# Optimization experiments

Hardware: AMD Instinct MI355X
Metric: run time of the kernel (lower is better)

## Reference

```python
import jax, jax.numpy as jnp
import numpy as np

B, S, D = 4, 2048, 1024


def setup_inputs() -> dict:
    key = jax.random.key(0)
    k1, k2, k3, k4 = jax.random.split(key, 4)
    x = jax.random.normal(k1, (B, S, D), dtype=jnp.float32)
    # 'random_normal' keras initializer uses stddev=0.05
    w_keys = jax.random.normal(k2, (D, D), dtype=jnp.float32) * 0.05
    w_queries = jax.random.normal(k3, (D, D), dtype=jnp.float32) * 0.05
    w_values = jax.random.normal(k4, (D, D), dtype=jnp.float32) * 0.05
    return {"x": x, "w_keys": w_keys, "w_queries": w_queries, "w_values": w_values}


def reference(x, w_keys, w_queries, w_values):
    # fact = sqrt(input feature dim)
    fact = jnp.sqrt(jnp.asarray(x.shape[-1], x.dtype))
    vk = x @ w_keys      # [B,S,D]
    vq = x @ w_queries   # [B,S,D]
    vv = x @ w_values    # [B,S,D]
    # NOTE: module computes K @ Q^T (keys as rows), softmax over last axis
    kq = jnp.einsum('bsd,btd->bst', vk, vq) / fact   # [B,S,S]
    sn = jax.nn.softmax(kq, axis=-1)
    # pm + transpose_b cancel: out = sn @ vv
    out = jnp.einsum('bst,btd->bsd', sn, vv)         # [B,S,D]
    return out
```

## Files before the change

kernel.cpp:

```cpp
#include <hip/hip_runtime.h>


typedef __attribute__((ext_vector_type(8))) short bf16x8;
typedef __attribute__((ext_vector_type(4))) float f32x4;

__device__ __forceinline__ unsigned short f2bf(float f) {
    unsigned int u = __float_as_uint(f);
    u += 0x7fff + ((u >> 16) & 1);
    return (unsigned short)(u >> 16);
}
__device__ __forceinline__ float bf2f(unsigned short s) {
    return __uint_as_float((unsigned int)s << 16);
}

__device__ __forceinline__ void gld_lds16(const unsigned short* g, unsigned short* l) {
    __builtin_amdgcn_global_load_lds(
        (const __attribute__((address_space(1))) void*)g,
        (__attribute__((address_space(3))) void*)l, 16, 0, 0);
}

template<int N> __device__ __forceinline__ void vmcnt_wait() {
    if constexpr (N == 0) asm volatile("s_waitcnt vmcnt(0)" ::: "memory");
    else if constexpr (N == 3) asm volatile("s_waitcnt vmcnt(3)" ::: "memory");
    else if constexpr (N == 4) asm volatile("s_waitcnt vmcnt(4)" ::: "memory");
}
__device__ __forceinline__ void bar() {
    asm volatile("" ::: "memory");
    __builtin_amdgcn_s_barrier();
    asm volatile("" ::: "memory");
}

template<int BN, int KT, bool RS>
__device__ __forceinline__ void gemm8(
    const unsigned short* __restrict__ A, const unsigned short* __restrict__ B,
    int lda, int ldb, int bm, int bn,
    unsigned short* As, unsigned short* Bs,
    f32x4 (&acc)[8][BN/64], float (&rs)[8])
{
    constexpr int NFR = BN / 64, NH = NFR / 2, LB = BN / 128;
    const int tid  = threadIdx.x;
    const int lane = tid & 63;
    const int wave = tid >> 6;
    const int wr = wave >> 2, wc = wave & 3;
    const int lr = lane & 15, kg = lane >> 4;

    const int srow = tid >> 2;
    const int soff = ((tid & 3) ^ ((tid >> 3) & 3)) * 8;
    const unsigned short* pa0 = A + (size_t)(bm + srow) * lda + soff;
    const unsigned short* pa1 = A + (size_t)(bm + 128 + srow) * lda + soff;
    const unsigned short* pb0 = B + (size_t)(bn + srow) * ldb + soff;
    const unsigned short* pb1 = B + (size_t)(bn + 128 + srow) * ldb + soff;

    const int runit = (kg ^ ((lr >> 1) & 3)) * 8;
    const int arow  = (wr * 128 + lr) * 32 + runit;
    const int brow  = (wc * (BN / 4) + lr) * 32 + runit;

    auto stageA = [&](int buf, int kt, int kh) {
        unsigned short* d = As + buf * 16384 + kh * 8192 + wave * 512;
        const int off = kt * 64 + kh * 32;
        gld_lds16(pa0 + off, d);
        gld_lds16(pa1 + off, d + 4096);
    };
    auto stageB = [&](int buf, int kt, int kh) {
        unsigned short* d = Bs + buf * (BN * 64) + kh * (BN * 32) + wave * 512;
        const int off = kt * 64 + kh * 32;
        gld_lds16(pb0 + off, d);
        if constexpr (BN == 256) gld_lds16(pb1 + off, d + 4096);
    };

    stageA(0, 0, 0); stageB(0, 0, 0); stageA(0, 0, 1); stageB(0, 0, 1);
    vmcnt_wait<0>();
    bar();

    for (int kt = 0; kt < KT; ++kt) {
        const int c = kt & 1, n = c ^ 1;
        const bool last = (kt == KT - 1);
        const unsigned short* Ab = As + c * 16384 + arow;
        const unsigned short* Bb = Bs + c * (BN * 64) + brow;

        bf16x8 af[8], bfr[NH];
        #pragma unroll
        for (int mf = 0; mf < 8; mf++) af[mf] = *reinterpret_cast<const bf16x8*>(Ab + mf * 512);
        #pragma unroll
        for (int j = 0; j < NH; j++) bfr[j] = *reinterpret_cast<const bf16x8*>(Bb + j * 512);
        if (!last) stageA(n, kt + 1, 0);
        bar();
        __builtin_amdgcn_s_setprio(1);
        #pragma unroll
        for (int mf = 0; mf < 8; mf++)
            #pragma unroll
            for (int j = 0; j < NH; j++)
                acc[mf][j] = __builtin_amdgcn_mfma_f32_16x16x32_bf16(af[mf], bfr[j], acc[mf][j], 0, 0, 0);
        __builtin_amdgcn_s_setprio(0);
        if constexpr (RS) {
            #pragma unroll
            for (int mf = 0; mf < 8; mf++)
                #pragma unroll
                for (int e = 0; e < 8; e++) rs[mf] += bf2f(((unsigned short*)&af[mf])[e]);
        }
        bar();

        #pragma unroll
        for (int j = 0; j < NH; j++) bfr[j] = *reinterpret_cast<const bf16x8*>(Bb + (NH + j) * 512);
        if (!last) stageB(n, kt + 1, 0);
        if (last) vmcnt_wait<0>(); else vmcnt_wait<2 + LB>();
        bar();
        __builtin_amdgcn_s_setprio(1);
        #pragma unroll
        for (int mf = 0; mf < 8; mf++)
            #pragma unroll
            for (int j = 0; j < NH; j++)
                acc[mf][NH + j] = __builtin_amdgcn_mfma_f32_16x16x32_bf16(af[mf], bfr[j], acc[mf][NH + j], 0, 0, 0);
        __builtin_amdgcn_s_setprio(0);
        bar();

        #pragma unroll
        for (int mf = 0; mf < 8; mf++) af[mf] = *reinterpret_cast<const bf16x8*>(Ab + 8192 + mf * 512);
        #pragma unroll
        for (int j = 0; j < NH; j++) bfr[j] = *reinterpret_cast<const bf16x8*>(Bb + BN * 32 + j * 512);
        if (!last) stageA(n, kt + 1, 1);
        bar();
        __builtin_amdgcn_s_setprio(1);
        #pragma unroll
        for (int mf = 0; mf < 8; mf++)
            #pragma unroll
            for (int j = 0; j < NH; j++)
                acc[mf][j] = __builtin_amdgcn_mfma_f32_16x16x32_bf16(af[mf], bfr[j], acc[mf][j], 0, 0, 0);
        __builtin_amdgcn_s_setprio(0);
        if constexpr (RS) {
            #pragma unroll
            for (int mf = 0; mf < 8; mf++)
                #pragma unroll
                for (int e = 0; e < 8; e++) rs[mf] += bf2f(((unsigned short*)&af[mf])[e]);
        }
        bar();

        #pragma unroll
        for (int j = 0; j < NH; j++) bfr[j] = *reinterpret_cast<const bf16x8*>(Bb + BN * 32 + (NH + j) * 512);
        if (!last) { stageB(n, kt + 1, 1); vmcnt_wait<2 + LB>(); }
        bar();
        __builtin_amdgcn_s_setprio(1);
        #pragma unroll
        for (int mf = 0; mf < 8; mf++)
            #pragma unroll
            for (int j = 0; j < NH; j++)
                acc[mf][NH + j] = __builtin_amdgcn_mfma_f32_16x16x32_bf16(af[mf], bfr[j], acc[mf][NH + j], 0, 0, 0);
        __builtin_amdgcn_s_setprio(0);
        bar();
    }
}

__global__ __launch_bounds__(256) void convert_x(
    const float* __restrict__ x, unsigned short* __restrict__ xb)
{
    const size_t idx = (size_t)blockIdx.x * 256 + threadIdx.x;
    const float4* xi = reinterpret_cast<const float4*>(x) + idx * 2;
    float4 v0 = xi[0], v1 = xi[1];
    ushort4 a = { f2bf(v0.x), f2bf(v0.y), f2bf(v0.z), f2bf(v0.w) };
    ushort4 b = { f2bf(v1.x), f2bf(v1.y), f2bf(v1.z), f2bf(v1.w) };
    ushort4* xo = reinterpret_cast<ushort4*>(xb) + idx * 2;
    xo[0] = a; xo[1] = b;
}

__global__ __launch_bounds__(256) void transpose_w(
    const float* __restrict__ w0, const float* __restrict__ w1, const float* __restrict__ w2,
    unsigned short* __restrict__ wT)
{
    __shared__ unsigned short T[64][72];
    const int z = blockIdx.z;
    const float* w = (z == 0) ? w0 : (z == 1 ? w1 : w2);
    unsigned short* o = wT + (size_t)z * 1024 * 1024;
    const int k0 = blockIdx.y * 64, n0 = blockIdx.x * 64;
    const int tid = threadIdx.x;
    const int r = tid >> 4, c4 = (tid & 15) * 4;
    #pragma unroll
    for (int i = 0; i < 4; i++) {
        int kr = r + i * 16;
        float4 v = *reinterpret_cast<const float4*>(&w[(size_t)(k0 + kr) * 1024 + n0 + c4]);
        T[c4 + 0][kr] = f2bf(v.x);
        T[c4 + 1][kr] = f2bf(v.y);
        T[c4 + 2][kr] = f2bf(v.z);
        T[c4 + 3][kr] = f2bf(v.w);
    }
    __syncthreads();
    #pragma unroll
    for (int i = 0; i < 4; i++) {
        int n = r + i * 16;
        ushort4 v = *reinterpret_cast<const ushort4*>(&T[n][c4]);
        *reinterpret_cast<ushort4*>(&o[(size_t)(n0 + n) * 1024 + k0 + c4]) = v;
    }
}

__global__ __launch_bounds__(512, 2) void proj_gemm(
    const unsigned short* __restrict__ xb, const unsigned short* __restrict__ wT,
    unsigned short* __restrict__ vk, unsigned short* __restrict__ vq,
    unsigned short* __restrict__ vvT)
{
    __shared__ unsigned short As[2 * 256 * 64], Bs[2 * 128 * 64];
    const int bid = blockIdx.x;
    const int wg  = (bid & 7) * 96 + (bid >> 3);
    const int z   = wg >> 8;
    const int rem = wg & 255;
    const int bm  = (rem >> 3) * 256;
    const int bn  = (rem & 7) * 128;
    const unsigned short* Bw = wT + (size_t)z * 1024 * 1024;

    f32x4 acc[8][2] = {};
    float rs[8] = {};
    gemm8<128, 16, false>(xb, Bw, 1024, 1024, bm, bn, As, Bs, acc, rs);

    const int tid = threadIdx.x, lane = tid & 63, wave = tid >> 6;
    const int wr = wave >> 2, wc = wave & 3, lr = lane & 15, kg = lane >> 4;
    if (z < 2) {
        unsigned short* out = z ? vq : vk;
        #pragma unroll
        for (int mf = 0; mf < 8; mf++)
            #pragma unroll
            for (int nf = 0; nf < 2; nf++)
                #pragma unroll
                for (int r = 0; r < 4; r++)
                    out[(size_t)(bm + wr * 128 + mf * 16 + kg * 4 + r) * 1024
                        + bn + wc * 32 + nf * 16 + lr] = f2bf(acc[mf][nf][r]);
    } else {
        const int batch = bm >> 11;
        unsigned short* o = vvT + (size_t)batch * 1024 * 2048;
        #pragma unroll
        for (int mf = 0; mf < 8; mf++)
            #pragma unroll
            for (int nf = 0; nf < 2; nf++) {
                ushort4 v = { f2bf(acc[mf][nf][0]), f2bf(acc[mf][nf][1]),
                              f2bf(acc[mf][nf][2]), f2bf(acc[mf][nf][3]) };
                *reinterpret_cast<ushort4*>(
                    &o[(size_t)(bn + wc * 32 + nf * 16 + lr) * 2048
                       + (bm & 2047) + wr * 128 + mf * 16 + kg * 4]) = v;
            }
    }
}

__global__ __launch_bounds__(512, 2) void scores_gemm(
    const unsigned short* __restrict__ vk, const unsigned short* __restrict__ vq,
    unsigned short* __restrict__ P)
{
    __shared__ unsigned short As[2 * 256 * 64], Bs[2 * 256 * 64];
    const int bid = blockIdx.x;
    const int wg  = (bid & 7) * 32 + (bid >> 3);
    const int z   = wg >> 6;
    const int rem = wg & 63;
    const int bm  = (rem >> 3) * 256;
    const int bn  = (rem & 7) * 256;
    const unsigned short* A = vk + (size_t)z * 2048 * 1024;
    const unsigned short* B = vq + (size_t)z * 2048 * 1024;
    unsigned short* out = P + (size_t)z * 2048 * 2048;

    f32x4 acc[8][4] = {};
    float rs[8] = {};
    gemm8<256, 16, false>(A, B, 1024, 1024, bm, bn, As, Bs, acc, rs);

    const int tid = threadIdx.x, lane = tid & 63, wave = tid >> 6;
    const int wr = wave >> 2, wc = wave & 3, lr = lane & 15, kg = lane >> 4;
    #pragma unroll
    for (int mf = 0; mf < 8; mf++)
        #pragma unroll
        for (int nf = 0; nf < 4; nf++)
            #pragma unroll
            for (int r = 0; r < 4; r++)
                out[(size_t)(bm + wr * 128 + mf * 16 + kg * 4 + r) * 2048
                    + bn + wc * 64 + nf * 16 + lr]
                    = f2bf(__expf(acc[mf][nf][r] * 0.03125f));
}

__global__ __launch_bounds__(512, 2) void pv_gemm(
    const unsigned short* __restrict__ P, const unsigned short* __restrict__ vvT,
    float* __restrict__ out)
{
    __shared__ unsigned short As[2 * 256 * 64], Bs[2 * 128 * 64];
    const int bid = blockIdx.x;
    const int wg  = (bid & 7) * 32 + (bid >> 3);
    const int z   = wg >> 6;
    const int rem = wg & 63;
    const int bm  = (rem >> 3) * 256;
    const int bn  = (rem & 7) * 128;
    const unsigned short* A = P   + (size_t)z * 2048 * 2048;
    const unsigned short* B = vvT + (size_t)z * 1024 * 2048;
    float* o = out + (size_t)z * 2048 * 1024;

    f32x4 acc[8][2] = {};
    float rs[8] = {};
    gemm8<128, 32, true>(A, B, 2048, 2048, bm, bn, As, Bs, acc, rs);

    const int tid = threadIdx.x, lane = tid & 63, wave = tid >> 6;
    const int wr = wave >> 2, wc = wave & 3, lr = lane & 15, kg = lane >> 4;

    #pragma unroll
    for (int mf = 0; mf < 8; mf++) {
        rs[mf] += __shfl_xor(rs[mf], 16);
        rs[mf] += __shfl_xor(rs[mf], 32);
    }
    #pragma unroll
    for (int mf = 0; mf < 8; mf++)
        #pragma unroll
        for (int r = 0; r < 4; r++) {
            const float l = __shfl(rs[mf], kg * 4 + r);
            const float inv = 1.0f / l;
            #pragma unroll
            for (int nf = 0; nf < 2; nf++)
                o[(size_t)(bm + wr * 128 + mf * 16 + kg * 4 + r) * 1024
                  + bn + wc * 32 + nf * 16 + lr] = acc[mf][nf][r] * inv;
        }
}

extern "C" void kernel_launch(void* const* d_in, const int* in_sizes, int n_in,
                              void* d_out, int out_size, void* d_ws, size_t ws_size,
                              hipStream_t stream) {
    const float* x  = (const float*)d_in[0];
    const float* wk = (const float*)d_in[1];
    const float* wq = (const float*)d_in[2];
    const float* wv = (const float*)d_in[3];
    float* out = (float*)d_out;

    char* ws = (char*)d_ws;
    const size_t MB = 1024 * 1024;
    unsigned short* xb  = (unsigned short*)(ws);
    unsigned short* wT  = (unsigned short*)(ws + 16 * MB);
    unsigned short* P   = (unsigned short*)(ws);
    unsigned short* vk  = (unsigned short*)(ws + 64 * MB);
    unsigned short* vq  = (unsigned short*)(ws + 80 * MB);
    unsigned short* vvT = (unsigned short*)(ws + 96 * MB);

    convert_x  <<<dim3(4096),      256, 0, stream>>>(x, xb);
    transpose_w<<<dim3(16, 16, 3), 256, 0, stream>>>(wk, wq, wv, wT);
    proj_gemm  <<<dim3(768),       512, 0, stream>>>(xb, wT, vk, vq, vvT);
    scores_gemm<<<dim3(256),       512, 0, stream>>>(vk, vq, P);
    pv_gemm    <<<dim3(256),       512, 0, stream>>>(P, vvT, out);
}
```

Baseline: 191.7 us.

## Restructure GEMM mainloop to prefetch two k-tiles ahead with fewer barriers

Replaces the four-phase interleaved mainloop, which had separate A/B staging and a barrier around every MFMA quarter, with a single stage call per k-step that loads both A and B. The tile for kt+2 is prefetched into the buffer just consumed, and only the kt+1 tile is waited on. This reduces the barrier count per k-step from eight to two and deepens the effective global-load lookahead. In exchange, all B fragments are held at once, which raises register pressure, and the global loads issue in bursts instead of being spread between MFMA groups.

```diff
diff --git a/kernel.cpp b/kernel.cpp
--- a/kernel.cpp
+++ b/kernel.cpp
@@ -21,8 +21,11 @@
 
 template<int N> __device__ __forceinline__ void vmcnt_wait() {
     if constexpr (N == 0) asm volatile("s_waitcnt vmcnt(0)" ::: "memory");
-    else if constexpr (N == 3) asm volatile("s_waitcnt vmcnt(3)" ::: "memory");
-    else if constexpr (N == 4) asm volatile("s_waitcnt vmcnt(4)" ::: "memory");
+    else if constexpr (N == 6) asm volatile("s_waitcnt vmcnt(6)" ::: "memory");
+    else if constexpr (N == 8) asm volatile("s_waitcnt vmcnt(8)" ::: "memory");
+}
+__device__ __forceinline__ void lgkm0() {
+    asm volatile("s_waitcnt lgkmcnt(0)" ::: "memory");
 }
 __device__ __forceinline__ void bar() {
     asm volatile("" ::: "memory");
@@ -37,7 +40,9 @@
     unsigned short* As, unsigned short* Bs,
     f32x4 (&acc)[8][BN/64], float (&rs)[8])
 {
-    constexpr int NFR = BN / 64, NH = NFR / 2, LB = BN / 128;
+    constexpr int NFR = BN / 64;
+    constexpr int LB  = BN / 128;
+    constexpr int L   = 4 + 2 * LB;
     const int tid  = threadIdx.x;
     const int lane = tid & 63;
     const int wave = tid >> 6;
@@ -55,97 +60,63 @@
     const int arow  = (wr * 128 + lr) * 32 + runit;
     const int brow  = (wc * (BN / 4) + lr) * 32 + runit;
 
-    auto stageA = [&](int buf, int kt, int kh) {
-        unsigned short* d = As + buf * 16384 + kh * 8192 + wave * 512;
-        const int off = kt * 64 + kh * 32;
-        gld_lds16(pa0 + off, d);
-        gld_lds16(pa1 + off, d + 4096);
+    auto stage = [&](int buf, int kt) {
+        unsigned short* da = As + buf * 16384 + wave * 512;
+        unsigned short* db = Bs + buf * (BN * 64) + wave * 512;
+        const int o0 = kt * 64, o1 = kt * 64 + 32;
+        gld_lds16(pa0 + o0, da);
+        gld_lds16(pa1 + o0, da + 4096);
+        gld_lds16(pa0 + o1, da + 8192);
+        gld_lds16(pa1 + o1, da + 8192 + 4096);
+        gld_lds16(pb0 + o0, db);
+        if constexpr (BN == 256) gld_lds16(pb1 + o0, db + 4096);
+        gld_lds16(pb0 + o1, db + BN * 32);
+        if constexpr (BN == 256) gld_lds16(pb1 + o1, db + BN * 32 + 4096);
     };
-    auto stageB = [&](int buf, int kt, int kh) {
-        unsigned short* d = Bs + buf * (BN * 64) + kh * (BN * 32) + wave * 512;
-        const int off = kt * 64 + kh * 32;
-        gld_lds16(pb0 + off, d);
-        if constexpr (BN == 256) gld_lds16(pb1 + off, d + 4096);
-    };
-
-    stageA(0, 0, 0); stageB(0, 0, 0); stageA(0, 0, 1); stageB(0, 0, 1);
-    vmcnt_wait<0>();
+
+    stage(0, 0);
+    stage(1, 1);
+    vmcnt_wait<L>();
     bar();
 
     for (int kt = 0; kt < KT; ++kt) {
-        const int c = kt & 1, n = c ^ 1;
-        const bool last = (kt == KT - 1);
+        const int c = kt & 1;
         const unsigned short* Ab = As + c * 16384 + arow;
         const unsigned short* Bb = Bs + c * (BN * 64) + brow;
 
-        bf16x8 af[8], bfr[NH];
-        #pragma unroll
-        for (int mf = 0; mf < 8; mf++) af[mf] = *reinterpret_cast<const bf16x8*>(Ab + mf * 512);
-        #pragma unroll
-        for (int j = 0; j < NH; j++) bfr[j] = *reinterpret_cast<const bf16x8*>(Bb + j * 512);
-        if (!last) stageA(n, kt + 1, 0);
-        bar();
-        __builtin_amdgcn_s_setprio(1);
-        #pragma unroll
-        for (int mf = 0; mf < 8; mf++)
-            #pragma unroll
-            for (int j = 0; j < NH; j++)
-                acc[mf][j] = __builtin_amdgcn_mfma_f32_16x16x32_bf16(af[mf], bfr[j], acc[mf][j], 0, 0, 0);
-        __builtin_amdgcn_s_setprio(0);
-        if constexpr (RS) {
+        #pragma unroll
+        for (int kk = 0; kk < 2; kk++) {
+            bf16x8 af[8], bfr[NFR];
+            #pragma unroll
+            for (int mf = 0; mf < 8; mf++)
+                af[mf] = *reinterpret_cast<const bf16x8*>(Ab + kk * 8192 + mf * 512);
+            #pragma unroll
+            for (int nf = 0; nf < NFR; nf++)
+                bfr[nf] = *reinterpret_cast<const bf16x8*>(Bb + kk * BN * 32 + nf * 512);
+            __builtin_amdgcn_s_setprio(1);
             #pragma unroll
             for (int mf = 0; mf < 8; mf++)
                 #pragma unroll
-                for (int e = 0; e < 8; e++) rs[mf] += bf2f(((unsigned short*)&af[mf])[e]);
+                for (int nf = 0; nf < NFR; nf++)
+                    acc[mf][nf] = __builtin_amdgcn_mfma_f32_16x16x32_bf16(af[mf], bfr[nf], acc[mf][nf], 0, 0, 0);
+            __builtin_amdgcn_s_setprio(0);
+            if constexpr (RS) {
+                #pragma unroll
+                for (int mf = 0; mf < 8; mf++)
+                    #pragma unroll
+                    for (int e = 0; e < 8; e++) rs[mf] += bf2f(((unsigned short*)&af[mf])[e]);
+            }
         }
+
+        if (kt == KT - 1) break;
+        lgkm0();
         bar();
-
-        #pragma unroll
-        for (int j = 0; j < NH; j++) bfr[j] = *reinterpret_cast<const bf16x8*>(Bb + (NH + j) * 512);
-        if (!last) stageB(n, kt + 1, 0);
-        if (last) vmcnt_wait<0>(); else vmcnt_wait<2 + LB>();
-        bar();
-        __builtin_amdgcn_s_setprio(1);
-        #pragma unroll
-        for (int mf = 0; mf < 8; mf++)
-            #pragma unroll
-            for (int j = 0; j < NH; j++)
-                acc[mf][NH + j] = __builtin_amdgcn_mfma_f32_16x16x32_bf16(af[mf], bfr[j], acc[mf][NH + j], 0, 0, 0);
-        __builtin_amdgcn_s_setprio(0);
-        bar();
-
-        #pragma unroll
-        for (int mf = 0; mf < 8; mf++) af[mf] = *reinterpret_cast<const bf16x8*>(Ab + 8192 + mf * 512);
-        #pragma unroll
-        for (int j = 0; j < NH; j++) bfr[j] = *reinterpret_cast<const bf16x8*>(Bb + BN * 32 + j * 512);
-        if (!last) stageA(n, kt + 1, 1);
-        bar();
-        __builtin_amdgcn_s_setprio(1);
-        #pragma unroll
-        for (int mf = 0; mf < 8; mf++)
-            #pragma unroll
-            for (int j = 0; j < NH; j++)
-                acc[mf][j] = __builtin_amdgcn_mfma_f32_16x16x32_bf16(af[mf], bfr[j], acc[mf][j], 0, 0, 0);
-        __builtin_amdgcn_s_setprio(0);
-        if constexpr (RS) {
-            #pragma unroll
-            for (int mf = 0; mf < 8; mf++)
-                #pragma unroll
-                for (int e = 0; e < 8; e++) rs[mf] += bf2f(((unsigned short*)&af[mf])[e]);
+        if (kt + 2 < KT) {
+            stage(c, kt + 2);
+            vmcnt_wait<L>();
+        } else {
+            vmcnt_wait<0>();
         }
-        bar();
-
-        #pragma unroll
-        for (int j = 0; j < NH; j++) bfr[j] = *reinterpret_cast<const bf16x8*>(Bb + BN * 32 + (NH + j) * 512);
-        if (!last) { stageB(n, kt + 1, 1); vmcnt_wait<2 + LB>(); }
-        bar();
-        __builtin_amdgcn_s_setprio(1);
-        #pragma unroll
-        for (int mf = 0; mf < 8; mf++)
-            #pragma unroll
-            for (int j = 0; j < NH; j++)
-                acc[mf][NH + j] = __builtin_amdgcn_mfma_f32_16x16x32_bf16(af[mf], bfr[j], acc[mf][NH + j], 0, 0, 0);
-        __builtin_amdgcn_s_setprio(0);
         bar();
     }
 }
```

New measurement: 211.5 us. 1.1x slower.
